# Performance work log

Hardware: AMD Instinct MI355X
Metric: run time of the kernel (lower is better)

The kernel has to match this reference:

```python
import jax, jax.numpy as jnp
import numpy as np

B, H, S, E = 4, 16, 4096, 128


def setup_inputs() -> dict:
    key = jax.random.key(0)
    k1, k2 = jax.random.split(key)
    x = jax.random.normal(k1, (B, H, S, E), dtype=jnp.float32)
    coord_positions = jnp.arange(S, dtype=jnp.float32)
    S_cayley = 0.01 * jax.random.normal(k2, (E, E), dtype=jnp.float32)
    return {"x": x, "coord_positions": coord_positions, "S_cayley": S_cayley}


def reference(x, coord_positions, S_cayley):
    embed_dim = x.shape[-1]
    # Cayley transform: P = (I + A)^{-1} (I - A), A antisymmetric -> P orthogonal
    A = (S_cayley - S_cayley.T) / 2.0
    I = jnp.eye(embed_dim, dtype=x.dtype)
    P = jnp.linalg.solve(I + A, I - A)
    # Learned orthogonal projection applied to every token vector
    xt = jnp.matmul(x, P.T)  # (B, H, S, E)
    # RoPE-style rotation with rotate-half convention
    freqs = 1.0 / 10000 ** (jnp.arange(0, embed_dim // 2, dtype=jnp.float32) * 2 / embed_dim)
    angles = jnp.outer(coord_positions, freqs)          # (S, E/2)
    cos_vals = jnp.repeat(jnp.cos(angles), 2, axis=-1)  # (S, E)
    sin_vals = jnp.repeat(jnp.sin(angles), 2, axis=-1)  # (S, E)
    x1, x2 = jnp.split(xt, 2, axis=-1)
    x_perm = jnp.concatenate([-x2, x1], axis=-1)
    return xt * cos_vals[None, None, :, :] + x_perm * sin_vals[None, None, :, :]
```

## Files before the change

### kernel.cpp

```cpp
#include <hip/hip_runtime.h>
#include <hip/hip_bf16.h>
#include <cstdint>
#include <cstddef>

#define S_LEN 4096
#define E_DIM 128
#define NROWS (4 * 16 * 4096)
#define GRID_MAIN 1024
#define ITERS 4

typedef __attribute__((ext_vector_type(8))) short bh8;
typedef __attribute__((ext_vector_type(4))) short s4;
typedef __attribute__((ext_vector_type(4))) float f4;
typedef unsigned short u16;

__device__ __forceinline__ u16 f2bf(float f) {
    union { float f; uint32_t u; } v; v.f = f;
    uint32_t r = v.u + 0x7FFFu + ((v.u >> 16) & 1u);
    return (u16)(r >> 16);
}
__device__ __forceinline__ short bfc(float f) {
    __hip_bfloat16 h = __float2bfloat16(f);
    return *reinterpret_cast<short*>(&h);
}
__device__ __forceinline__ float bf2f(u16 u) {
    union { uint32_t u; float f; } v; v.u = ((uint32_t)u) << 16;
    return v.f;
}

__device__ __forceinline__ bh8 ldsRow(const u16* M, int row, int c) {
    return *(const bh8*)(&M[row * 128 + ((c ^ (row & 15)) * 8)]);
}
__device__ __forceinline__ int swzIdx(int n, int m) {
    return n * 128 + (((m >> 3) ^ (n & 15)) * 8) + (m & 7);
}

__global__ __launch_bounds__(1024) void k_pro(const float* __restrict__ Sc,
        const float* __restrict__ pos, u16* __restrict__ Qb,
        float* __restrict__ csT) {
    if (blockIdx.x != 0) {
        int t = (blockIdx.x - 1) * 1024 + threadIdx.x;
        for (int e = t; e < S_LEN * 64; e += 16 * 1024) {
            int s = e >> 6, f = e & 63;
            float freq = exp2f(-0.20762050593046015f * (float)f);
            float sv, cv;
            sincosf(pos[s] * freq, &sv, &cv);
            csT[s * 128 + 2 * f]     = cv;
            csT[s * 128 + 2 * f + 1] = sv;
        }
        return;
    }
    __shared__ u16 Abf[128 * 128];
    __shared__ u16 A2bf[128 * 128];
    __shared__ u16 Y1bf[128 * 128];
    __shared__ u16 A4bf[128 * 128];

    for (int e = threadIdx.x; e < 16384; e += 1024) {
        int i = e >> 7, j = e & 127;
        float a = 0.5f * (Sc[i * 128 + j] - Sc[j * 128 + i]);
        Abf[swzIdx(i, j)] = f2bf(a);
    }
    __syncthreads();

    const int wave = threadIdx.x >> 6;
    const int lane = threadIdx.x & 63;
    const int lhi = lane >> 4, llo = lane & 15;
    const int sm = wave & 7;
    const int nh = wave >> 3;

    {
        f4 acc[4];
        #pragma unroll
        for (int t = 0; t < 4; ++t) { f4 z = {0.f,0.f,0.f,0.f}; acc[t] = z; }
        #pragma unroll
        for (int kk = 0; kk < 4; ++kk) {
            bh8 yf = ldsRow(Abf, sm * 16 + llo, kk * 4 + lhi);
            #pragma unroll
            for (int t = 0; t < 4; ++t) {
                bh8 xf = ldsRow(Abf, (nh * 4 + t) * 16 + llo, kk * 4 + lhi);
                acc[t] = __builtin_amdgcn_mfma_f32_16x16x32_bf16(xf, yf, acc[t], 0, 0, 0);
            }
        }
        __syncthreads();
        #pragma unroll
        for (int t = 0; t < 4; ++t)
            #pragma unroll
            for (int r = 0; r < 4; ++r) {
                int n = (nh * 4 + t) * 16 + lhi * 4 + r, m = sm * 16 + llo;
                float a2 = -acc[t][r];
                A2bf[swzIdx(n, m)] = f2bf(a2);
                Y1bf[swzIdx(n, m)] = f2bf(a2 + bf2f(Abf[swzIdx(n, m)]));
            }
    }
    __syncthreads();
    {
        f4 acc[4];
        #pragma unroll
        for (int t = 0; t < 4; ++t) { f4 z = {0.f,0.f,0.f,0.f}; acc[t] = z; }
        #pragma unroll
        for (int kk = 0; kk < 4; ++kk) {
            bh8 yf = ldsRow(A2bf, sm * 16 + llo, kk * 4 + lhi);
            #pragma unroll
            for (int t = 0; t < 4; ++t) {
                bh8 xf = ldsRow(A2bf, (nh * 4 + t) * 16 + llo, kk * 4 + lhi);
                acc[t] = __builtin_amdgcn_mfma_f32_16x16x32_bf16(xf, yf, acc[t], 0, 0, 0);
            }
        }
        #pragma unroll
        for (int t = 0; t < 4; ++t)
            #pragma unroll
            for (int r = 0; r < 4; ++r) {
                int n = (nh * 4 + t) * 16 + lhi * 4 + r, m = sm * 16 + llo;
                A4bf[swzIdx(n, m)] = f2bf(acc[t][r]);
            }
    }
    __syncthreads();
    {
        f4 acc[4];
        #pragma unroll
        for (int t = 0; t < 4; ++t) { f4 z = {0.f,0.f,0.f,0.f}; acc[t] = z; }
        #pragma unroll
        for (int kk = 0; kk < 4; ++kk) {
            bh8 yf = ldsRow(Y1bf, sm * 16 + llo, kk * 4 + lhi);
            #pragma unroll
            for (int t = 0; t < 4; ++t) {
                bh8 xf = ldsRow(A2bf, (nh * 4 + t) * 16 + llo, kk * 4 + lhi);
                acc[t] = __builtin_amdgcn_mfma_f32_16x16x32_bf16(xf, yf, acc[t], 0, 0, 0);
            }
        }
        #pragma unroll
        for (int kk = 0; kk < 4; ++kk) {
            bh8 yf = ldsRow(Y1bf, sm * 16 + llo, kk * 4 + lhi);
            #pragma unroll
            for (int t = 0; t < 4; ++t) {
                bh8 xf = ldsRow(A4bf, (nh * 4 + t) * 16 + llo, kk * 4 + lhi);
                acc[t] = __builtin_amdgcn_mfma_f32_16x16x32_bf16(xf, yf, acc[t], 0, 0, 0);
            }
        }
        #pragma unroll
        for (int t = 0; t < 4; ++t)
            #pragma unroll
            for (int r = 0; r < 4; ++r) {
                int n = (nh * 4 + t) * 16 + lhi * 4 + r, m = sm * 16 + llo;
                float q = 2.0f * (acc[t][r] + bf2f(A2bf[swzIdx(n, m)])
                                            - bf2f(Abf[swzIdx(n, m)]));
                Qb[n * 128 + m] = f2bf(q);
            }
    }
}

__global__ __launch_bounds__(256, 3) void k_main(const float* __restrict__ x,
        const u16* __restrict__ Qb, const float* __restrict__ csT,
        float* __restrict__ out) {
    __shared__ u16 Plds[128 * 128];
    __shared__ u16 scr[4][16 * 128];

    const int wave = threadIdx.x >> 6;
    const int lane = threadIdx.x & 63;
    const int lhi = lane >> 4, llo = lane & 15;
    const int half = lane >> 5, c = lane & 31;
    const int s0 = blockIdx.x * ITERS;
    const int bh_lane = wave * 16 + llo;

    f4 xs[8];
    #pragma unroll
    for (int j = 0; j < 8; ++j) {
        const int bh = wave * 16 + 2 * j + half;
        xs[j] = *(const f4*)(x + ((size_t)bh * S_LEN + s0) * E_DIM + 4 * c);
    }

    #pragma unroll
    for (int i = 0; i < 8; ++i) {
        int chunk = i * 256 + threadIdx.x;
        int row = chunk >> 4, cc = chunk & 15;
        int pc = cc ^ (row & 15);
        bh8 v = *(const bh8*)(Qb + chunk * 8);
        *(bh8*)(&Plds[row * 128 + pc * 8]) = v;
    }
    __syncthreads();

    u16* myscr = scr[wave];

    #pragma unroll 1
    for (int it = 0; it < ITERS; ++it) {
        const int s = s0 + it;

        f4 xsn[8];
        if (it + 1 < ITERS) {
            #pragma unroll
            for (int j = 0; j < 8; ++j) {
                const int bh = wave * 16 + 2 * j + half;
                xsn[j] = *(const f4*)(x + ((size_t)bh * S_LEN + s + 1) * E_DIM + 4 * c);
            }
        } else {
            #pragma unroll
            for (int j = 0; j < 8; ++j) xsn[j] = xs[j];
        }
        __builtin_amdgcn_sched_barrier(0);

        #pragma unroll
        for (int j = 0; j < 8; ++j) {
            const int tok = 2 * j + half;
            s4 v;
            v[0] = bfc(xs[j][0]); v[1] = bfc(xs[j][1]);
            v[2] = bfc(xs[j][2]); v[3] = bfc(xs[j][3]);
            *(s4*)(&myscr[tok * 128 + (((c >> 1) ^ tok) & 15) * 8 + (c & 1) * 4]) = v;
        }

        f4 acc[8];
        #pragma unroll
        for (int t = 0; t < 8; ++t) { f4 z = {0.f, 0.f, 0.f, 0.f}; acc[t] = z; }
        #pragma unroll
        for (int kk = 0; kk < 4; ++kk) {
            const int pc = (kk * 4 + lhi) ^ llo;
            bh8 frag = *(const bh8*)(&myscr[llo * 128 + (pc & 15) * 8]);
            #pragma unroll
            for (int t = 0; t < 8; ++t) {
                bh8 qfrag = *(const bh8*)(&Plds[(t * 16 + llo) * 128 + pc * 8]);
                acc[t] = __builtin_amdgcn_mfma_f32_16x16x32_bf16(qfrag, frag, acc[t], 0, 0, 0);
            }
        }
        __builtin_amdgcn_sched_barrier(0);

        f4 cs_lo[4], cs_hi[4];
        const float* csp = csT + (size_t)s * 128;
        #pragma unroll
        for (int t = 0; t < 4; ++t) {
            cs_lo[t] = *(const f4*)(csp + t * 16 + lhi * 4);
            cs_hi[t] = *(const f4*)(csp + 64 + t * 16 + lhi * 4);
        }

        float* orow = out + ((size_t)bh_lane * S_LEN + s) * E_DIM;
        #pragma unroll
        for (int t = 0; t < 4; ++t) {
            const int n0 = t * 16 + lhi * 4;
            const int ch_lo = t * 2 + (lhi >> 1);
            const int ch_hi = ch_lo + 8;
            s4 xb_lo = *(const s4*)(&myscr[llo * 128 + ((ch_lo ^ llo) & 15) * 8 + (lhi & 1) * 4]);
            s4 xb_hi = *(const s4*)(&myscr[llo * 128 + ((ch_hi ^ llo) & 15) * 8 + (lhi & 1) * 4]);
            f4 olo, ohi;
            #pragma unroll
            for (int r = 0; r < 4; ++r) {
                float xt1 = acc[t][r]     + bf2f((u16)xb_lo[r]);
                float xt2 = acc[t + 4][r] + bf2f((u16)xb_hi[r]);
                float c1 = cs_lo[t][(r >> 1) * 2], s1 = cs_lo[t][(r >> 1) * 2 + 1];
                float c2 = cs_hi[t][(r >> 1) * 2], s2 = cs_hi[t][(r >> 1) * 2 + 1];
                olo[r] = xt1 * c1 - xt2 * s1;
                ohi[r] = xt2 * c2 + xt1 * s2;
            }
            *(f4*)(orow + n0) = olo;
            *(f4*)(orow + n0 + 64) = ohi;
        }

        #pragma unroll
        for (int j = 0; j < 8; ++j) xs[j] = xsn[j];
    }
}

extern "C" void kernel_launch(void* const* d_in, const int* in_sizes, int n_in,
                              void* d_out, int out_size, void* d_ws, size_t ws_size,
                              hipStream_t stream) {
    const float* x   = (const float*)d_in[0];
    const float* pos = (const float*)d_in[1];
    const float* Sc  = (const float*)d_in[2];
    float* out = (float*)d_out;

    char* ws = (char*)d_ws;
    u16* Qb     = (u16*)(ws);
    float* csT  = (float*)(ws + 32768);

    k_pro<<<17, 1024, 0, stream>>>(Sc, pos, Qb, csT);
    k_main<<<GRID_MAIN, 256, 0, stream>>>(x, Qb, csT, out);
}
```

Baseline: 74.97 us.

## Compute RoPE sin/cos inline and process contiguous token rows with deeper prefetch

Drops the precomputed cos/sin table and its producer blocks in the prologue kernel. Angles are now computed inline with the hardware v_sin/v_cos instructions on range-reduced revolutions, and the upper-half frequencies are derived from the lower half by a factor of 0.01. The main kernel now maps each wave to 16 consecutive flattened (bh, s) rows rather than a strided set of bh rows at one position, which makes loads and stores contiguous. It also keeps two input buffers in flight to prefetch two iterations ahead. The trade-offs are extra per-thread transcendental work, lower angle accuracy at large positions, and higher register pressure.

```diff
diff --git a/kernel.cpp b/kernel.cpp
--- a/kernel.cpp
+++ b/kernel.cpp
@@ -27,6 +27,11 @@
     union { uint32_t u; float f; } v; v.u = ((uint32_t)u) << 16;
     return v.f;
 }
+__device__ __forceinline__ void fsincos(float rev, float& sv, float& cv) {
+    float r = rev - floorf(rev);
+    asm("v_sin_f32 %0, %1" : "=v"(sv) : "v"(r));
+    asm("v_cos_f32 %0, %1" : "=v"(cv) : "v"(r));
+}
 
 __device__ __forceinline__ bh8 ldsRow(const u16* M, int row, int c) {
     return *(const bh8*)(&M[row * 128 + ((c ^ (row & 15)) * 8)]);
@@ -36,20 +41,7 @@
 }
 
 __global__ __launch_bounds__(1024) void k_pro(const float* __restrict__ Sc,
-        const float* __restrict__ pos, u16* __restrict__ Qb,
-        float* __restrict__ csT) {
-    if (blockIdx.x != 0) {
-        int t = (blockIdx.x - 1) * 1024 + threadIdx.x;
-        for (int e = t; e < S_LEN * 64; e += 16 * 1024) {
-            int s = e >> 6, f = e & 63;
-            float freq = exp2f(-0.20762050593046015f * (float)f);
-            float sv, cv;
-            sincosf(pos[s] * freq, &sv, &cv);
-            csT[s * 128 + 2 * f]     = cv;
-            csT[s * 128 + 2 * f + 1] = sv;
-        }
-        return;
-    }
+        u16* __restrict__ Qb) {
     __shared__ u16 Abf[128 * 128];
     __shared__ u16 A2bf[128 * 128];
     __shared__ u16 Y1bf[128 * 128];
@@ -149,24 +141,101 @@
     }
 }
 
+__device__ __forceinline__ void iter_body(int it, f4 (&xs)[8],
+        const float* __restrict__ x, const float* __restrict__ pos,
+        float* __restrict__ out, const u16* Plds, u16* myscr,
+        const float (&frev)[8], int wbase0, int half, int c, int lhi, int llo) {
+    const int wbase = wbase0 + it * 64;
+    const int m = wbase + llo;
+    const int s = m & (S_LEN - 1);
+    const float p = pos[s];
+
+    #pragma unroll
+    for (int j = 0; j < 8; ++j) {
+        const int tok = 2 * j + half;
+        const int q = c >> 1;
+        s4 v;
+        v[0] = bfc(xs[j][0]); v[1] = bfc(xs[j][1]);
+        v[2] = bfc(xs[j][2]); v[3] = bfc(xs[j][3]);
+        *(s4*)(&myscr[tok * 128 + ((q ^ tok) & 15) * 8 + (c & 1) * 4]) = v;
+    }
+    __builtin_amdgcn_sched_barrier(0);
+
+    f4 acc[8];
+    #pragma unroll
+    for (int t = 0; t < 8; ++t) { f4 z = {0.f, 0.f, 0.f, 0.f}; acc[t] = z; }
+    #pragma unroll
+    for (int kk = 0; kk < 4; ++kk) {
+        const int pc = (kk * 4 + lhi) ^ llo;
+        bh8 frag = *(const bh8*)(&myscr[llo * 128 + pc * 8]);
+        #pragma unroll
+        for (int t = 0; t < 8; ++t) {
+            bh8 qfrag = *(const bh8*)(&Plds[(t * 16 + llo) * 128 + pc * 8]);
+            acc[t] = __builtin_amdgcn_mfma_f32_16x16x32_bf16(qfrag, frag, acc[t], 0, 0, 0);
+        }
+    }
+    __builtin_amdgcn_sched_barrier(0);
+
+    float* orow = out + (size_t)m * E_DIM;
+    #pragma unroll
+    for (int t = 0; t < 4; ++t) {
+        const int n0 = t * 16 + lhi * 4;
+        const int q_lo = t * 2 + (lhi >> 1);
+        const int sub = (lhi & 1) * 4;
+        s4 xbl = *(const s4*)(&myscr[llo * 128 + ((q_lo ^ llo) & 15) * 8 + sub]);
+        s4 xbh = *(const s4*)(&myscr[llo * 128 + (((q_lo + 8) ^ llo) & 15) * 8 + sub]);
+        float sa0, ca0, sa1, ca1, sh0, ch0, sh1, ch1;
+        float r0 = p * frev[t * 2], r1 = p * frev[t * 2 + 1];
+        fsincos(r0, sa0, ca0);
+        fsincos(r1, sa1, ca1);
+        fsincos(r0 * 0.01f, sh0, ch0);
+        fsincos(r1 * 0.01f, sh1, ch1);
+        f4 olo, ohi;
+        #pragma unroll
+        for (int r = 0; r < 4; ++r) {
+            float xt1 = acc[t][r]     + bf2f((u16)xbl[r]);
+            float xt2 = acc[t + 4][r] + bf2f((u16)xbh[r]);
+            float cv = (r < 2) ? ca0 : ca1, sv = (r < 2) ? sa0 : sa1;
+            float cvh = (r < 2) ? ch0 : ch1, svh = (r < 2) ? sh0 : sh1;
+            olo[r] = xt1 * cv - xt2 * sv;
+            ohi[r] = xt2 * cvh + xt1 * svh;
+        }
+        *(f4*)(orow + n0) = olo;
+        *(f4*)(orow + n0 + 64) = ohi;
+    }
+    __builtin_amdgcn_sched_barrier(0);
+
+    if (it + 2 < ITERS) {
+        const float* xb = x + (size_t)(wbase + 128) * E_DIM;
+        #pragma unroll
+        for (int j = 0; j < 8; ++j)
+            xs[j] = *(const f4*)(xb + (2 * j + half) * E_DIM + 4 * c);
+    }
+}
+
 __global__ __launch_bounds__(256, 3) void k_main(const float* __restrict__ x,
-        const u16* __restrict__ Qb, const float* __restrict__ csT,
+        const u16* __restrict__ Qb, const float* __restrict__ pos,
         float* __restrict__ out) {
     __shared__ u16 Plds[128 * 128];
     __shared__ u16 scr[4][16 * 128];
 
     const int wave = threadIdx.x >> 6;
     const int lane = threadIdx.x & 63;
-    const int lhi = lane >> 4, llo = lane & 15;
-    const int half = lane >> 5, c = lane & 31;
-    const int s0 = blockIdx.x * ITERS;
-    const int bh_lane = wave * 16 + llo;
-
-    f4 xs[8];
-    #pragma unroll
-    for (int j = 0; j < 8; ++j) {
-        const int bh = wave * 16 + 2 * j + half;
-        xs[j] = *(const f4*)(x + ((size_t)bh * S_LEN + s0) * E_DIM + 4 * c);
+    const int lhi = (lane >> 4) & 3, llo = lane & 15;
+    const int half = lane >> 5;
+    const int c = lane & 31;
+    const int wbase0 = blockIdx.x * (64 * ITERS) + wave * 16;
+
+    f4 xsA[8], xsB[8];
+    {
+        const float* xb = x + (size_t)wbase0 * E_DIM;
+        #pragma unroll
+        for (int j = 0; j < 8; ++j)
+            xsA[j] = *(const f4*)(xb + (2 * j + half) * E_DIM + 4 * c);
+        const float* xb1 = x + (size_t)(wbase0 + 64) * E_DIM;
+        #pragma unroll
+        for (int j = 0; j < 8; ++j)
+            xsB[j] = *(const f4*)(xb1 + (2 * j + half) * E_DIM + 4 * c);
     }
 
     #pragma unroll
@@ -177,83 +246,22 @@
         bh8 v = *(const bh8*)(Qb + chunk * 8);
         *(bh8*)(&Plds[row * 128 + pc * 8]) = v;
     }
+
+    float frev[8];
+    #pragma unroll
+    for (int t = 0; t < 4; ++t)
+        #pragma unroll
+        for (int b = 0; b < 2; ++b)
+            frev[t * 2 + b] = exp2f(-0.20762050593046015f * (float)(t * 8 + lhi * 2 + b))
+                              * 0.15915494309189535f;
+
     __syncthreads();
 
     u16* myscr = scr[wave];
-
     #pragma unroll 1
-    for (int it = 0; it < ITERS; ++it) {
-        const int s = s0 + it;
-
-        f4 xsn[8];
-        if (it + 1 < ITERS) {
-            #pragma unroll
-            for (int j = 0; j < 8; ++j) {
-                const int bh = wave * 16 + 2 * j + half;
-                xsn[j] = *(const f4*)(x + ((size_t)bh * S_LEN + s + 1) * E_DIM + 4 * c);
-            }
-        } else {
-            #pragma unroll
-            for (int j = 0; j < 8; ++j) xsn[j] = xs[j];
-        }
-        __builtin_amdgcn_sched_barrier(0);
-
-        #pragma unroll
-        for (int j = 0; j < 8; ++j) {
-            const int tok = 2 * j + half;
-            s4 v;
-            v[0] = bfc(xs[j][0]); v[1] = bfc(xs[j][1]);
-            v[2] = bfc(xs[j][2]); v[3] = bfc(xs[j][3]);
-            *(s4*)(&myscr[tok * 128 + (((c >> 1) ^ tok) & 15) * 8 + (c & 1) * 4]) = v;
-        }
-
-        f4 acc[8];
-        #pragma unroll
-        for (int t = 0; t < 8; ++t) { f4 z = {0.f, 0.f, 0.f, 0.f}; acc[t] = z; }
-        #pragma unroll
-        for (int kk = 0; kk < 4; ++kk) {
-            const int pc = (kk * 4 + lhi) ^ llo;
-            bh8 frag = *(const bh8*)(&myscr[llo * 128 + (pc & 15) * 8]);
-            #pragma unroll
-            for (int t = 0; t < 8; ++t) {
-                bh8 qfrag = *(const bh8*)(&Plds[(t * 16 + llo) * 128 + pc * 8]);
-                acc[t] = __builtin_amdgcn_mfma_f32_16x16x32_bf16(qfrag, frag, acc[t], 0, 0, 0);
-            }
-        }
-        __builtin_amdgcn_sched_barrier(0);
-
-        f4 cs_lo[4], cs_hi[4];
-        const float* csp = csT + (size_t)s * 128;
-        #pragma unroll
-        for (int t = 0; t < 4; ++t) {
-            cs_lo[t] = *(const f4*)(csp + t * 16 + lhi * 4);
-            cs_hi[t] = *(const f4*)(csp + 64 + t * 16 + lhi * 4);
-        }
-
-        float* orow = out + ((size_t)bh_lane * S_LEN + s) * E_DIM;
-        #pragma unroll
-        for (int t = 0; t < 4; ++t) {
-            const int n0 = t * 16 + lhi * 4;
-            const int ch_lo = t * 2 + (lhi >> 1);
-            const int ch_hi = ch_lo + 8;
-            s4 xb_lo = *(const s4*)(&myscr[llo * 128 + ((ch_lo ^ llo) & 15) * 8 + (lhi & 1) * 4]);
-            s4 xb_hi = *(const s4*)(&myscr[llo * 128 + ((ch_hi ^ llo) & 15) * 8 + (lhi & 1) * 4]);
-            f4 olo, ohi;
-            #pragma unroll
-            for (int r = 0; r < 4; ++r) {
-                float xt1 = acc[t][r]     + bf2f((u16)xb_lo[r]);
-                float xt2 = acc[t + 4][r] + bf2f((u16)xb_hi[r]);
-                float c1 = cs_lo[t][(r >> 1) * 2], s1 = cs_lo[t][(r >> 1) * 2 + 1];
-                float c2 = cs_hi[t][(r >> 1) * 2], s2 = cs_hi[t][(r >> 1) * 2 + 1];
-                olo[r] = xt1 * c1 - xt2 * s1;
-                ohi[r] = xt2 * c2 + xt1 * s2;
-            }
-            *(f4*)(orow + n0) = olo;
-            *(f4*)(orow + n0 + 64) = ohi;
-        }
-
-        #pragma unroll
-        for (int j = 0; j < 8; ++j) xs[j] = xsn[j];
+    for (int it2 = 0; it2 < ITERS; it2 += 2) {
+        iter_body(it2,     xsA, x, pos, out, Plds, myscr, frev, wbase0, half, c, lhi, llo);
+        iter_body(it2 + 1, xsB, x, pos, out, Plds, myscr, frev, wbase0, half, c, lhi, llo);
     }
 }
 
@@ -265,10 +273,8 @@
     const float* Sc  = (const float*)d_in[2];
     float* out = (float*)d_out;
 
-    char* ws = (char*)d_ws;
-    u16* Qb     = (u16*)(ws);
-    float* csT  = (float*)(ws + 32768);
-
-    k_pro<<<17, 1024, 0, stream>>>(Sc, pos, Qb, csT);
-    k_main<<<GRID_MAIN, 256, 0, stream>>>(x, Qb, csT, out);
-}
+    u16* Qb = (u16*)d_ws;
+
+    k_pro<<<1, 1024, 0, stream>>>(Sc, Qb);
+    k_main<<<GRID_MAIN, 256, 0, stream>>>(x, Qb, pos, out);
+}
```

Result: slower. 81.37 us (+8.5%).

## Remap tokens to contiguous rows and double-buffer x loads two iterations ahead

Applied to the files above, without the earlier changes.

Changes the work mapping so each wave handles 16 consecutive flattened rows rather than 16 (b,h) pairs at a single position, which makes x reads and output writes contiguous. The loop is fully unrolled through a template with two register buffers, so x loads are issued two iterations ahead. Each row now loads its own cos/sin entry. This targets load latency and scattered memory access, at the cost of more live registers under the 3-blocks-per-CU launch bound.

```diff
diff --git a/kernel.cpp b/kernel.cpp
--- a/kernel.cpp
+++ b/kernel.cpp
@@ -149,25 +149,79 @@
     }
 }
 
+template <int IT>
+__device__ __forceinline__ void iter_body(f4 (&xs)[8],
+        const float* __restrict__ x, const float* __restrict__ csT,
+        float* __restrict__ out, const u16* Plds, u16* myscr,
+        int wbase0, int half, int c, int lhi, int llo) {
+    const int wbase = wbase0 + IT * 64;
+    const int m = wbase + llo;
+    const int s = m & (S_LEN - 1);
+
+    #pragma unroll
+    for (int j = 0; j < 8; ++j) {
+        const int tok = 2 * j + half;
+        s4 v;
+        v[0] = bfc(xs[j][0]); v[1] = bfc(xs[j][1]);
+        v[2] = bfc(xs[j][2]); v[3] = bfc(xs[j][3]);
+        *(s4*)(&myscr[tok * 128 + (((c >> 1) ^ tok) & 15) * 8 + (c & 1) * 4]) = v;
+    }
+    __builtin_amdgcn_sched_barrier(0);
+
+    f4 acc[8];
+    #pragma unroll
+    for (int t = 0; t < 8; ++t) { f4 z = {0.f, 0.f, 0.f, 0.f}; acc[t] = z; }
+    #pragma unroll
+    for (int kk = 0; kk < 4; ++kk) {
+        const int pc = (kk * 4 + lhi) ^ llo;
+        bh8 frag = *(const bh8*)(&myscr[llo * 128 + pc * 8]);
+        #pragma unroll
+        for (int t = 0; t < 8; ++t) {
+            bh8 qfrag = *(const bh8*)(&Plds[(t * 16 + llo) * 128 + pc * 8]);
+            acc[t] = __builtin_amdgcn_mfma_f32_16x16x32_bf16(qfrag, frag, acc[t], 0, 0, 0);
+        }
+    }
+    __builtin_amdgcn_sched_barrier(0);
+
+    const float* csp = csT + (size_t)s * 128;
+    float* orow = out + (size_t)m * E_DIM;
+    #pragma unroll
+    for (int t = 0; t < 4; ++t) {
+        const int n0 = t * 16 + lhi * 4;
+        const int q_lo = t * 2 + (lhi >> 1);
+        const int sub = (lhi & 1) * 4;
+        s4 xbl = *(const s4*)(&myscr[llo * 128 + ((q_lo ^ llo) & 15) * 8 + sub]);
+        s4 xbh = *(const s4*)(&myscr[llo * 128 + (((q_lo + 8) ^ llo) & 15) * 8 + sub]);
+        f4 cs_lo = *(const f4*)(csp + n0);
+        f4 cs_hi = *(const f4*)(csp + 64 + n0);
+        f4 olo, ohi;
+        #pragma unroll
+        for (int r = 0; r < 4; ++r) {
+            float xt1 = acc[t][r]     + bf2f((u16)xbl[r]);
+            float xt2 = acc[t + 4][r] + bf2f((u16)xbh[r]);
+            float c1 = cs_lo[(r >> 1) * 2], s1 = cs_lo[(r >> 1) * 2 + 1];
+            float c2 = cs_hi[(r >> 1) * 2], s2 = cs_hi[(r >> 1) * 2 + 1];
+            olo[r] = xt1 * c1 - xt2 * s1;
+            ohi[r] = xt2 * c2 + xt1 * s2;
+        }
+        *(f4*)(orow + n0) = olo;
+        *(f4*)(orow + n0 + 64) = ohi;
+    }
+    __builtin_amdgcn_sched_barrier(0);
+
+    if constexpr (IT + 2 < ITERS) {
+        const float* xb = x + (size_t)(wbase + 128) * E_DIM;
+        #pragma unroll
+        for (int j = 0; j < 8; ++j)
+            xs[j] = *(const f4*)(xb + (2 * j + half) * E_DIM + 4 * c);
+    }
+}
+
 __global__ __launch_bounds__(256, 3) void k_main(const float* __restrict__ x,
         const u16* __restrict__ Qb, const float* __restrict__ csT,
         float* __restrict__ out) {
     __shared__ u16 Plds[128 * 128];
     __shared__ u16 scr[4][16 * 128];
-
-    const int wave = threadIdx.x >> 6;
-    const int lane = threadIdx.x & 63;
-    const int lhi = lane >> 4, llo = lane & 15;
-    const int half = lane >> 5, c = lane & 31;
-    const int s0 = blockIdx.x * ITERS;
-    const int bh_lane = wave * 16 + llo;
-
-    f4 xs[8];
-    #pragma unroll
-    for (int j = 0; j < 8; ++j) {
-        const int bh = wave * 16 + 2 * j + half;
-        xs[j] = *(const f4*)(x + ((size_t)bh * S_LEN + s0) * E_DIM + 4 * c);
-    }
 
     #pragma unroll
     for (int i = 0; i < 8; ++i) {
@@ -177,84 +231,33 @@
         bh8 v = *(const bh8*)(Qb + chunk * 8);
         *(bh8*)(&Plds[row * 128 + pc * 8]) = v;
     }
-    __syncthreads();
-
+
+    const int wave = threadIdx.x >> 6;
+    const int lane = threadIdx.x & 63;
+    const int lhi = (lane >> 4) & 3, llo = lane & 15;
+    const int half = lane >> 5;
+    const int c = lane & 31;
     u16* myscr = scr[wave];
 
-    #pragma unroll 1
-    for (int it = 0; it < ITERS; ++it) {
-        const int s = s0 + it;
-
-        f4 xsn[8];
-        if (it + 1 < ITERS) {
-            #pragma unroll
-            for (int j = 0; j < 8; ++j) {
-                const int bh = wave * 16 + 2 * j + half;
-                xsn[j] = *(const f4*)(x + ((size_t)bh * S_LEN + s + 1) * E_DIM + 4 * c);
-            }
-        } else {
-            #pragma unroll
-            for (int j = 0; j < 8; ++j) xsn[j] = xs[j];
-        }
-        __builtin_amdgcn_sched_barrier(0);
-
-        #pragma unroll
-        for (int j = 0; j < 8; ++j) {
-            const int tok = 2 * j + half;
-            s4 v;
-            v[0] = bfc(xs[j][0]); v[1] = bfc(xs[j][1]);
-            v[2] = bfc(xs[j][2]); v[3] = bfc(xs[j][3]);
-            *(s4*)(&myscr[tok * 128 + (((c >> 1) ^ tok) & 15) * 8 + (c & 1) * 4]) = v;
-        }
-
-        f4 acc[8];
-        #pragma unroll
-        for (int t = 0; t < 8; ++t) { f4 z = {0.f, 0.f, 0.f, 0.f}; acc[t] = z; }
-        #pragma unroll
-        for (int kk = 0; kk < 4; ++kk) {
-            const int pc = (kk * 4 + lhi) ^ llo;
-            bh8 frag = *(const bh8*)(&myscr[llo * 128 + (pc & 15) * 8]);
-            #pragma unroll
-            for (int t = 0; t < 8; ++t) {
-                bh8 qfrag = *(const bh8*)(&Plds[(t * 16 + llo) * 128 + pc * 8]);
-                acc[t] = __builtin_amdgcn_mfma_f32_16x16x32_bf16(qfrag, frag, acc[t], 0, 0, 0);
-            }
-        }
-        __builtin_amdgcn_sched_barrier(0);
-
-        f4 cs_lo[4], cs_hi[4];
-        const float* csp = csT + (size_t)s * 128;
-        #pragma unroll
-        for (int t = 0; t < 4; ++t) {
-            cs_lo[t] = *(const f4*)(csp + t * 16 + lhi * 4);
-            cs_hi[t] = *(const f4*)(csp + 64 + t * 16 + lhi * 4);
-        }
-
-        float* orow = out + ((size_t)bh_lane * S_LEN + s) * E_DIM;
-        #pragma unroll
-        for (int t = 0; t < 4; ++t) {
-            const int n0 = t * 16 + lhi * 4;
-            const int ch_lo = t * 2 + (lhi >> 1);
-            const int ch_hi = ch_lo + 8;
-            s4 xb_lo = *(const s4*)(&myscr[llo * 128 + ((ch_lo ^ llo) & 15) * 8 + (lhi & 1) * 4]);
-            s4 xb_hi = *(const s4*)(&myscr[llo * 128 + ((ch_hi ^ llo) & 15) * 8 + (lhi & 1) * 4]);
-            f4 olo, ohi;
-            #pragma unroll
-            for (int r = 0; r < 4; ++r) {
-                float xt1 = acc[t][r]     + bf2f((u16)xb_lo[r]);
-                float xt2 = acc[t + 4][r] + bf2f((u16)xb_hi[r]);
-                float c1 = cs_lo[t][(r >> 1) * 2], s1 = cs_lo[t][(r >> 1) * 2 + 1];
-                float c2 = cs_hi[t][(r >> 1) * 2], s2 = cs_hi[t][(r >> 1) * 2 + 1];
-                olo[r] = xt1 * c1 - xt2 * s1;
-                ohi[r] = xt2 * c2 + xt1 * s2;
-            }
-            *(f4*)(orow + n0) = olo;
-            *(f4*)(orow + n0 + 64) = ohi;
-        }
-
-        #pragma unroll
-        for (int j = 0; j < 8; ++j) xs[j] = xsn[j];
-    }
+    const int wbase0 = blockIdx.x * (64 * ITERS) + wave * 16;
+
+    f4 xsA[8], xsB[8];
+    {
+        const float* xb0 = x + (size_t)wbase0 * E_DIM;
+        const float* xb1 = xb0 + 64 * E_DIM;
+        #pragma unroll
+        for (int j = 0; j < 8; ++j)
+            xsA[j] = *(const f4*)(xb0 + (2 * j + half) * E_DIM + 4 * c);
+        #pragma unroll
+        for (int j = 0; j < 8; ++j)
+            xsB[j] = *(const f4*)(xb1 + (2 * j + half) * E_DIM + 4 * c);
+    }
+    __syncthreads();
+
+    iter_body<0>(xsA, x, csT, out, Plds, myscr, wbase0, half, c, lhi, llo);
+    iter_body<1>(xsB, x, csT, out, Plds, myscr, wbase0, half, c, lhi, llo);
+    iter_body<2>(xsA, x, csT, out, Plds, myscr, wbase0, half, c, lhi, llo);
+    iter_body<3>(xsB, x, csT, out, Plds, myscr, wbase0, half, c, lhi, llo);
 }
 
 extern "C" void kernel_launch(void* const* d_in, const int* in_sizes, int n_in,
```

Result: slower. 78.66 us (+4.9%).
